# Optimization experiments

Measured on AMD Instinct MI355X. Metric: run time of the kernel, lower is better.

Reference implementation:

```python
import jax, jax.numpy as jnp
import numpy as np


def _rx(state, theta, axis):
    # Apply RX(theta) to qubit at tensor axis `axis`. state: (B, 2,...,2) complex.
    half = theta * 0.5
    c = jnp.cos(half)
    s = jnp.sin(half)
    a0 = jnp.take(state, 0, axis=axis)
    a1 = jnp.take(state, 1, axis=axis)
    return jnp.stack([c * a0 - 1j * s * a1, c * a1 - 1j * s * a0], axis=axis)


def _cnot(state, w):
    # CNOT with control wire w (axis w+1), target wire w+1 (axis w+2).
    c_ax = w + 1
    s0 = jnp.take(state, 0, axis=c_ax)
    # after removing the control axis, the target axis index becomes c_ax
    s1 = jnp.flip(jnp.take(state, 1, axis=c_ax), axis=c_ax)
    return jnp.stack([s0, s1], axis=c_ax)


def _run_circuit(x, params):
    # x: (B, n) encoding angles; params: (depth, n) trainable RX angles.
    B, n = x.shape
    depth = params.shape[0]
    state = jnp.zeros((B,) + (2,) * n, jnp.complex64)
    state = state.at[(slice(None),) + (0,) * n].set(1.0 + 0.0j)
    # angle encoding: RX(x_w) on each wire
    for w in range(n):
        theta = x[:, w].reshape((B,) + (1,) * (n - 1))
        state = _rx(state, theta, w + 1)
    # variational layers: RX(param) per wire, then CNOT chain
    for d in range(depth):
        for w in range(n):
            state = _rx(state, params[d, w], w + 1)
        for w in range(n - 1):
            state = _cnot(state, w)
    probs = state.real ** 2 + state.imag ** 2  # (B, 2,...,2)
    ez = []
    for w in range(n):
        axes = tuple(a for a in range(1, n + 1) if a != w + 1)
        p = probs.sum(axes)  # (B, 2)
        ez.append(p[:, 0] - p[:, 1])  # <Z_w>
    return jnp.stack(ez, axis=1)  # (B, n)


def setup_inputs() -> dict:
    key = jax.random.key(0)
    k0, k1, k2, k3, k4 = jax.random.split(key, 5)
    seq_len, batch, input_dim = 256, 128, 64
    n_qubits, depth, hidden = 10, 2, 256
    inputs = jax.random.normal(k0, (seq_len, batch, input_dim), jnp.float32)
    mask = jax.random.randint(k1, (seq_len, batch), 0, 2).astype(jnp.int32)
    qparams = jax.random.normal(k2, (4, depth, n_qubits), jnp.float32)
    W = jax.random.normal(k3, (4, hidden, n_qubits), jnp.float32) / np.sqrt(n_qubits)
    b = jax.random.normal(k4, (4, hidden), jnp.float32) * 0.01
    return {"inputs": inputs, "mask": mask, "qparams": qparams, "W": W, "b": b}


def reference(inputs, mask, qparams, W, b):
    seq_len, batch, _ = inputs.shape
    n = qparams.shape[-1]
    hidden = W.shape[1]
    maskf = mask.astype(inputs.dtype)

    circuits4 = jax.vmap(_run_circuit, in_axes=(None, 0))  # over the 4 gates

    def step(carry, xm):
        hx, cx = carry
        x_t, m_t = xm
        q_in = jnp.concatenate([x_t, hx], axis=1)[:, :n]  # (B, n)
        z = circuits4(q_in, qparams)                      # (4, B, n)
        pre = jnp.einsum('gbn,ghn->gbh', z, W) + b[:, None, :]
        f = jax.nn.sigmoid(pre[0])
        i = jax.nn.sigmoid(pre[1])
        g = jnp.tanh(pre[2])
        o = jax.nn.sigmoid(pre[3])
        m = m_t[:, None]
        f = f * m + (1.0 - m)
        i = i * m
        g = g * m
        o = o * m + (1.0 - m)
        cx_new = f * cx + i * g
        hx_new = o * jnp.tanh(cx_new)
        return (hx_new, cx_new), hx_new

    h0 = jnp.zeros((batch, hidden), inputs.dtype)
    c0 = jnp.zeros((batch, hidden), inputs.dtype)
    (hx, cx), outputs = jax.lax.scan(jax.checkpoint(step), (h0, c0), (inputs, maskf))
    return outputs, (hx, cx)
```

## Files before the change

kernel.cpp:

```cpp
#include <hip/hip_runtime.h>

#define T_LEN 256
#define BATCH 128
#define NQ 10
#define HID 256
#define OUT_HX (T_LEN * BATCH * HID)
#define OUT_CX (OUT_HX + BATCH * HID)
#define ZSTRIDE 40
#define ZROW 44
#define TROW 65

#define KS  (-1.44269504089f)
#define KT2 (-2.88539008178f)

__global__ __launch_bounds__(256) void zker(
    const float* __restrict__ inputs,
    const float* __restrict__ qparams,
    float* __restrict__ zws)
{
  const int b   = blockIdx.x;
  const int tq  = blockIdx.y;
  const int tid = threadIdx.x;
  const int t   = tq * 64 + (tid >> 2);
  const int g   = tid & 3;

  const float sg = (g == 2) ? KT2 : KS;

  float th0[NQ], cth[NQ], sth[NQ];
#pragma unroll
  for (int k = 0; k < NQ; ++k) {
    th0[k]   = qparams[g * 2 * NQ + k];
    float t1 = qparams[g * 2 * NQ + NQ + k];
    sth[k] = __sinf(t1);
    cth[k] = __cosf(t1);
  }
  float cphi[NQ], sphi[NQ];
  const float* xp = inputs + (t * BATCH + b) * 64;
#pragma unroll
  for (int k = 0; k < NQ; ++k) {
    float ang = xp[k] + th0[k];
    sphi[k] = __sinf(ang);
    cphi[k] = __cosf(ang);
  }
  float* zout = zws + (b * T_LEN + t) * ZSTRIDE + g;
#pragma unroll
  for (int w = 0; w < NQ; ++w) {
    float vI, vZ, vY, vX; int js;
    if (w == NQ - 1) { vI = 0.f; vZ = cth[NQ-1]; vY = sth[NQ-1]; vX = 0.f; js = NQ - 2; }
    else             { vI = 1.f; vZ = 0.f; vY = 0.f; vX = 0.f; js = w; }
#pragma unroll
    for (int j = js; j >= 0; --j) {
      float nI = cth[j] * (cphi[j+1] * vZ - sphi[j+1] * vY);
      float nZ = cth[j] * vI;
      float nY = sth[j] * vX;
      float nX = -sth[j] * (sphi[j+1] * vZ + cphi[j+1] * vY);
      vI = nI; vZ = nZ; vY = nY; vX = nX;
    }
    zout[w * 4] = (vI + cphi[0] * vZ - sphi[0] * vY) * sg;
  }
}

__global__ __launch_bounds__(512) void scanker(
    const float* __restrict__ zws,
    const int*  __restrict__ mask,
    const float* __restrict__ W,
    const float* __restrict__ bias,
    float* __restrict__ out)
{
  const int b    = blockIdx.x;
  const int h0   = blockIdx.y * 64;
  const int tid  = threadIdx.x;
  const int lane = tid & 63;
  const int wavu = __builtin_amdgcn_readfirstlane(tid >> 6);

  __shared__ float zlds[T_LEN * ZROW];
  __shared__ float tlds[64 * TROW];
  __shared__ float mk[T_LEN];

  {
    const float4* zg = (const float4*)(zws + b * T_LEN * ZSTRIDE);
    for (int i = tid; i < T_LEN * 10; i += 512) {
      int t = i / 10, c4 = i - t * 10;
      *(float4*)&zlds[t * ZROW + c4 * 4] = zg[i];
    }
  }
  for (int t = tid; t < T_LEN; t += 512) mk[t] = (float)mask[t * BATCH + b];
  __syncthreads();

  int srcA[6];
#pragma unroll
  for (int k = 0; k < 6; ++k) {
    const int d = 1 << k;
    srcA[k] = ((lane >= d) ? (lane - d) : lane) << 2;
  }

  float bsc[8][4];
#pragma unroll
  for (int hh = 0; hh < 8; ++hh) {
    const int h = h0 + wavu * 8 + hh;
    bsc[hh][0] = bias[0 * HID + h] * KS;
    bsc[hh][1] = bias[1 * HID + h] * KS;
    bsc[hh][2] = bias[2 * HID + h] * KT2;
    bsc[hh][3] = bias[3 * HID + h] * KS;
  }

  float carry[8];
#pragma unroll
  for (int i = 0; i < 8; ++i) carry[i] = 0.f;

  for (int r = 0; r < 4; ++r) {
    const int t = r * 64 + lane;
    float4 z4[10];
#pragma unroll
    for (int n = 0; n < NQ; ++n) z4[n] = *(const float4*)&zlds[t * ZROW + n * 4];
    const float m = mk[t];
    const float onem = 1.f - m;

    float a8[8], w8[8], om8[8];
#pragma unroll
    for (int hh = 0; hh < 8; ++hh) {
      const int h = h0 + wavu * 8 + hh;
      const int wb = __builtin_amdgcn_readfirstlane(h * NQ);

      float p0 = bsc[hh][0];
      float p1 = bsc[hh][1];
      float p2 = bsc[hh][2];
      float p3 = bsc[hh][3];
#pragma unroll
      for (int n = 0; n < NQ; ++n) {
        p0 = fmaf(z4[n].x, W[0 * HID * NQ + wb + n], p0);
        p1 = fmaf(z4[n].y, W[1 * HID * NQ + wb + n], p1);
        p2 = fmaf(z4[n].z, W[2 * HID * NQ + wb + n], p2);
        p3 = fmaf(z4[n].w, W[3 * HID * NQ + wb + n], p3);
      }
      const float uf = __builtin_amdgcn_rcpf(1.f + __builtin_amdgcn_exp2f(p0));
      const float ui = __builtin_amdgcn_rcpf(1.f + __builtin_amdgcn_exp2f(p1));
      const float ug = __builtin_amdgcn_rcpf(1.f + __builtin_amdgcn_exp2f(p2));
      const float uo = __builtin_amdgcn_rcpf(1.f + __builtin_amdgcn_exp2f(p3));

      a8[hh]  = fmaf(m, uf, onem);
      w8[hh]  = m * ui * fmaf(2.f, ug, -1.f);
      om8[hh] = fmaf(m, uo, onem);
    }

#pragma unroll
    for (int k = 0; k < 6; ++k) {
      const int d = 1 << k;
      const bool p = (lane >= d);
#pragma unroll
      for (int hh = 0; hh < 8; ++hh) {
        float au = __int_as_float(
            __builtin_amdgcn_ds_bpermute(srcA[k], __float_as_int(a8[hh])));
        float wu = __int_as_float(
            __builtin_amdgcn_ds_bpermute(srcA[k], __float_as_int(w8[hh])));
        au = p ? au : 1.f;
        wu = p ? wu : 0.f;
        w8[hh] = fmaf(a8[hh], wu, w8[hh]);
        a8[hh] = a8[hh] * au;
      }
    }

#pragma unroll
    for (int hh = 0; hh < 8; ++hh) {
      const float ct = fmaf(a8[hh], carry[hh], w8[hh]);
      carry[hh] = __shfl(ct, 63, 64);

      const float ec = __builtin_amdgcn_exp2f(ct * KT2);
      const float tc = fmaf(2.f, __builtin_amdgcn_rcpf(1.f + ec), -1.f);
      const float hv = om8[hh] * tc;

      tlds[lane * TROW + wavu * 8 + hh] = hv;

      if (r == 3 && lane == 63) {
        const int h = h0 + wavu * 8 + hh;
        out[OUT_HX + b * HID + h] = hv;
        out[OUT_CX + b * HID + h] = ct;
      }
    }
    __syncthreads();
#pragma unroll
    for (int s = 0; s < 2; ++s) {
      const int q = tid + s * 512;
      const int tt = q >> 4, c = q & 15;
      float4 v;
      v.x = tlds[tt * TROW + 4 * c + 0];
      v.y = tlds[tt * TROW + 4 * c + 1];
      v.z = tlds[tt * TROW + 4 * c + 2];
      v.w = tlds[tt * TROW + 4 * c + 3];
      *(float4*)&out[(r * 64 + tt) * (BATCH * HID) + b * HID + h0 + 4 * c] = v;
    }
    __syncthreads();
  }
}

extern "C" void kernel_launch(void* const* d_in, const int* in_sizes, int n_in,
                              void* d_out, int out_size, void* d_ws, size_t ws_size,
                              hipStream_t stream)
{
  int ii = 0, im = 1, iq = 2, iw = 3, ib = 4;
  for (int i = 0; i < n_in; ++i) {
    switch (in_sizes[i]) {
      case 2097152: ii = i; break;
      case 32768:   im = i; break;
      case 80:      iq = i; break;
      case 10240:   iw = i; break;
      case 1024:    ib = i; break;
      default: break;
    }
  }
  const float* inputs  = (const float*)d_in[ii];
  const int*   mask    = (const int*)d_in[im];
  const float* qparams = (const float*)d_in[iq];
  const float* W       = (const float*)d_in[iw];
  const float* bias    = (const float*)d_in[ib];
  float*       out     = (float*)d_out;
  float*       zws     = (float*)d_ws;

  zker<<<dim3(BATCH, 4), dim3(256), 0, stream>>>(inputs, qparams, zws);
  scanker<<<dim3(BATCH, 4), dim3(512), 0, stream>>>(zws, mask, W, bias, out);
}
```

Before: 111.1 us.

## Split hidden dim across more blocks, stream z from global, double-buffer output LDS

Doubles the scan grid so each block handles 32 hidden units (4 per wave) instead of 64, which halves per-thread register work and bpermute traffic and raises the number of blocks. The z workspace is re-laid out as [b][qubit][t][gate], so the scan kernel reads float4s straight from global memory (coalesced per qubit) instead of staging them in LDS first. The output transpose buffer is double-buffered, which lets one of the two barriers per round be dropped. In exchange, each z row is now loaded by twice as many blocks, and per-lane global loads now sit inside the recurrence loop.

```diff
diff --git a/kernel.cpp b/kernel.cpp
--- a/kernel.cpp
+++ b/kernel.cpp
@@ -6,9 +6,7 @@
 #define HID 256
 #define OUT_HX (T_LEN * BATCH * HID)
 #define OUT_CX (OUT_HX + BATCH * HID)
-#define ZSTRIDE 40
-#define ZROW 44
-#define TROW 65
+#define TROW 33
 
 #define KS  (-1.44269504089f)
 #define KT2 (-2.88539008178f)
@@ -42,7 +40,7 @@
     sphi[k] = __sinf(ang);
     cphi[k] = __cosf(ang);
   }
-  float* zout = zws + (b * T_LEN + t) * ZSTRIDE + g;
+  float* zout = zws + (b * NQ * T_LEN + t) * 4 + g;
 #pragma unroll
   for (int w = 0; w < NQ; ++w) {
     float vI, vZ, vY, vX; int js;
@@ -56,7 +54,7 @@
       float nX = -sth[j] * (sphi[j+1] * vZ + cphi[j+1] * vY);
       vI = nI; vZ = nZ; vY = nY; vX = nX;
     }
-    zout[w * 4] = (vI + cphi[0] * vZ - sphi[0] * vY) * sg;
+    zout[w * T_LEN * 4] = (vI + cphi[0] * vZ - sphi[0] * vY) * sg;
   }
 }
 
@@ -68,128 +66,118 @@
     float* __restrict__ out)
 {
   const int b    = blockIdx.x;
-  const int h0   = blockIdx.y * 64;
+  const int h0   = blockIdx.y * 32;
   const int tid  = threadIdx.x;
   const int lane = tid & 63;
   const int wavu = __builtin_amdgcn_readfirstlane(tid >> 6);
 
-  __shared__ float zlds[T_LEN * ZROW];
-  __shared__ float tlds[64 * TROW];
+  __shared__ float tlds[2][64 * TROW];
   __shared__ float mk[T_LEN];
 
-  {
-    const float4* zg = (const float4*)(zws + b * T_LEN * ZSTRIDE);
-    for (int i = tid; i < T_LEN * 10; i += 512) {
-      int t = i / 10, c4 = i - t * 10;
-      *(float4*)&zlds[t * ZROW + c4 * 4] = zg[i];
-    }
-  }
   for (int t = tid; t < T_LEN; t += 512) mk[t] = (float)mask[t * BATCH + b];
   __syncthreads();
 
-  int srcA[6];
+  int srcA[6]; bool pm[6];
 #pragma unroll
   for (int k = 0; k < 6; ++k) {
     const int d = 1 << k;
+    pm[k]   = (lane >= d);
     srcA[k] = ((lane >= d) ? (lane - d) : lane) << 2;
   }
 
-  float bsc[8][4];
-#pragma unroll
-  for (int hh = 0; hh < 8; ++hh) {
-    const int h = h0 + wavu * 8 + hh;
+  float bsc[4][4];
+#pragma unroll
+  for (int hh = 0; hh < 4; ++hh) {
+    const int h = __builtin_amdgcn_readfirstlane(h0 + wavu * 4 + hh);
     bsc[hh][0] = bias[0 * HID + h] * KS;
     bsc[hh][1] = bias[1 * HID + h] * KS;
     bsc[hh][2] = bias[2 * HID + h] * KT2;
     bsc[hh][3] = bias[3 * HID + h] * KS;
   }
 
-  float carry[8];
-#pragma unroll
-  for (int i = 0; i < 8; ++i) carry[i] = 0.f;
+  float carry[4];
+#pragma unroll
+  for (int i = 0; i < 4; ++i) carry[i] = 0.f;
+
+  const float4* zg = (const float4*)zws + b * NQ * T_LEN;
 
   for (int r = 0; r < 4; ++r) {
+    const int p = r & 1;
     const int t = r * 64 + lane;
-    float4 z4[10];
-#pragma unroll
-    for (int n = 0; n < NQ; ++n) z4[n] = *(const float4*)&zlds[t * ZROW + n * 4];
     const float m = mk[t];
     const float onem = 1.f - m;
 
-    float a8[8], w8[8], om8[8];
-#pragma unroll
-    for (int hh = 0; hh < 8; ++hh) {
-      const int h = h0 + wavu * 8 + hh;
-      const int wb = __builtin_amdgcn_readfirstlane(h * NQ);
-
-      float p0 = bsc[hh][0];
-      float p1 = bsc[hh][1];
-      float p2 = bsc[hh][2];
-      float p3 = bsc[hh][3];
-#pragma unroll
-      for (int n = 0; n < NQ; ++n) {
-        p0 = fmaf(z4[n].x, W[0 * HID * NQ + wb + n], p0);
-        p1 = fmaf(z4[n].y, W[1 * HID * NQ + wb + n], p1);
-        p2 = fmaf(z4[n].z, W[2 * HID * NQ + wb + n], p2);
-        p3 = fmaf(z4[n].w, W[3 * HID * NQ + wb + n], p3);
+    float acc[4][4];
+#pragma unroll
+    for (int hh = 0; hh < 4; ++hh) {
+      acc[hh][0] = bsc[hh][0]; acc[hh][1] = bsc[hh][1];
+      acc[hh][2] = bsc[hh][2]; acc[hh][3] = bsc[hh][3];
+    }
+#pragma unroll
+    for (int n = 0; n < NQ; ++n) {
+      const float4 z = zg[n * T_LEN + t];
+#pragma unroll
+      for (int hh = 0; hh < 4; ++hh) {
+        const int wb = __builtin_amdgcn_readfirstlane((h0 + wavu * 4 + hh) * NQ + n);
+        acc[hh][0] = fmaf(z.x, W[0 * HID * NQ + wb], acc[hh][0]);
+        acc[hh][1] = fmaf(z.y, W[1 * HID * NQ + wb], acc[hh][1]);
+        acc[hh][2] = fmaf(z.z, W[2 * HID * NQ + wb], acc[hh][2]);
+        acc[hh][3] = fmaf(z.w, W[3 * HID * NQ + wb], acc[hh][3]);
       }
-      const float uf = __builtin_amdgcn_rcpf(1.f + __builtin_amdgcn_exp2f(p0));
-      const float ui = __builtin_amdgcn_rcpf(1.f + __builtin_amdgcn_exp2f(p1));
-      const float ug = __builtin_amdgcn_rcpf(1.f + __builtin_amdgcn_exp2f(p2));
-      const float uo = __builtin_amdgcn_rcpf(1.f + __builtin_amdgcn_exp2f(p3));
-
-      a8[hh]  = fmaf(m, uf, onem);
-      w8[hh]  = m * ui * fmaf(2.f, ug, -1.f);
-      om8[hh] = fmaf(m, uo, onem);
+    }
+
+    float a4[4], w4[4], om4[4];
+#pragma unroll
+    for (int hh = 0; hh < 4; ++hh) {
+      const float uf = __builtin_amdgcn_rcpf(1.f + __builtin_amdgcn_exp2f(acc[hh][0]));
+      const float ui = __builtin_amdgcn_rcpf(1.f + __builtin_amdgcn_exp2f(acc[hh][1]));
+      const float ug = __builtin_amdgcn_rcpf(1.f + __builtin_amdgcn_exp2f(acc[hh][2]));
+      const float uo = __builtin_amdgcn_rcpf(1.f + __builtin_amdgcn_exp2f(acc[hh][3]));
+      a4[hh]  = fmaf(m, uf, onem);
+      w4[hh]  = m * ui * fmaf(2.f, ug, -1.f);
+      om4[hh] = fmaf(m, uo, onem);
     }
 
 #pragma unroll
     for (int k = 0; k < 6; ++k) {
-      const int d = 1 << k;
-      const bool p = (lane >= d);
-#pragma unroll
-      for (int hh = 0; hh < 8; ++hh) {
+#pragma unroll
+      for (int hh = 0; hh < 4; ++hh) {
         float au = __int_as_float(
-            __builtin_amdgcn_ds_bpermute(srcA[k], __float_as_int(a8[hh])));
+            __builtin_amdgcn_ds_bpermute(srcA[k], __float_as_int(a4[hh])));
         float wu = __int_as_float(
-            __builtin_amdgcn_ds_bpermute(srcA[k], __float_as_int(w8[hh])));
-        au = p ? au : 1.f;
-        wu = p ? wu : 0.f;
-        w8[hh] = fmaf(a8[hh], wu, w8[hh]);
-        a8[hh] = a8[hh] * au;
+            __builtin_amdgcn_ds_bpermute(srcA[k], __float_as_int(w4[hh])));
+        au = pm[k] ? au : 1.f;
+        wu = pm[k] ? wu : 0.f;
+        w4[hh] = fmaf(a4[hh], wu, w4[hh]);
+        a4[hh] = a4[hh] * au;
       }
     }
 
 #pragma unroll
-    for (int hh = 0; hh < 8; ++hh) {
-      const float ct = fmaf(a8[hh], carry[hh], w8[hh]);
+    for (int hh = 0; hh < 4; ++hh) {
+      const float ct = fmaf(a4[hh], carry[hh], w4[hh]);
       carry[hh] = __shfl(ct, 63, 64);
-
       const float ec = __builtin_amdgcn_exp2f(ct * KT2);
       const float tc = fmaf(2.f, __builtin_amdgcn_rcpf(1.f + ec), -1.f);
-      const float hv = om8[hh] * tc;
-
-      tlds[lane * TROW + wavu * 8 + hh] = hv;
-
+      const float hv = om4[hh] * tc;
+      tlds[p][lane * TROW + wavu * 4 + hh] = hv;
       if (r == 3 && lane == 63) {
-        const int h = h0 + wavu * 8 + hh;
+        const int h = h0 + wavu * 4 + hh;
         out[OUT_HX + b * HID + h] = hv;
         out[OUT_CX + b * HID + h] = ct;
       }
     }
+
     __syncthreads();
-#pragma unroll
-    for (int s = 0; s < 2; ++s) {
-      const int q = tid + s * 512;
-      const int tt = q >> 4, c = q & 15;
+    {
+      const int tt = tid >> 3, c = tid & 7;
       float4 v;
-      v.x = tlds[tt * TROW + 4 * c + 0];
-      v.y = tlds[tt * TROW + 4 * c + 1];
-      v.z = tlds[tt * TROW + 4 * c + 2];
-      v.w = tlds[tt * TROW + 4 * c + 3];
+      v.x = tlds[p][tt * TROW + 4 * c + 0];
+      v.y = tlds[p][tt * TROW + 4 * c + 1];
+      v.z = tlds[p][tt * TROW + 4 * c + 2];
+      v.w = tlds[p][tt * TROW + 4 * c + 3];
       *(float4*)&out[(r * 64 + tt) * (BATCH * HID) + b * HID + h0 + 4 * c] = v;
     }
-    __syncthreads();
   }
 }
 
@@ -217,5 +205,5 @@
   float*       zws     = (float*)d_ws;
 
   zker<<<dim3(BATCH, 4), dim3(256), 0, stream>>>(inputs, qparams, zws);
-  scanker<<<dim3(BATCH, 4), dim3(512), 0, stream>>>(zws, mask, W, bias, out);
+  scanker<<<dim3(BATCH, 8), dim3(512), 0, stream>>>(zws, mask, W, bias, out);
 }
```

New measurement: 106.7 us. 4.0% less time.
